# Kernel optimization log

Hardware: AMD Instinct MI355X
Metric: run time of the kernel (lower is better)

The kernel has to match this reference:

```python
import jax, jax.numpy as jnp
import numpy as np

N, M = 100000, 800000
F_IN, F_E, H = 64, 16, 64
T_NODE, T_EDGE = 2, 3
HEAD_DIM = 16.0


def setup_inputs() -> dict:
    key = jax.random.key(0)
    ks = jax.random.split(key, 16)
    inp = {
        "x": jax.random.normal(ks[0], (N, F_IN), jnp.float32),
        "edge_feat": jax.random.normal(ks[1], (M, F_E), jnp.float32),
        "node_type": jax.random.randint(ks[2], (N,), 0, T_NODE, jnp.int32),
        "edge_src": jax.random.randint(ks[3], (M,), 0, N, jnp.int32),
        "edge_dst": jax.random.randint(ks[4], (M,), 0, N, jnp.int32),
        "edge_type": jax.random.randint(ks[5], (M,), 0, T_EDGE, jnp.int32),
    }
    s_n = 1.0 / np.sqrt(F_IN)
    s_e = 1.0 / np.sqrt(F_E)
    for i, name in enumerate(["W1", "W2", "W3", "W4"]):
        inp[name] = jax.random.normal(ks[6 + i], (T_NODE, F_IN, H), jnp.float32) * s_n
        inp["b" + name[1]] = jax.random.normal(ks[10 + i], (T_NODE, H), jnp.float32) * 0.01
    inp["W5"] = jax.random.normal(ks[14], (T_EDGE, F_E, H), jnp.float32) * s_e
    inp["b5"] = jax.random.normal(ks[15], (T_EDGE, H), jnp.float32) * 0.01
    return inp


def _node_proj(x, W, b, node_type):
    # per-node-type linear: [T,F,H] weights, select row per node type
    p = jnp.einsum('nf,tfh->tnh', x, W) + b[:, None, :]      # [T,N,H]
    return jnp.take_along_axis(p, node_type[None, :, None], axis=0)[0]  # [N,H]


def reference(x, edge_feat, W1, b1, W2, b2, W3, b3, W4, b4, W5, b5,
              node_type, edge_src, edge_dst, edge_type):
    n = x.shape[0]
    h1 = _node_proj(x, W1, b1, node_type)
    h2 = _node_proj(x, W2, b2, node_type)
    h3 = _node_proj(x, W3, b3, node_type)
    h4 = _node_proj(x, W4, b4, node_type)
    # per-edge-type linear via weight gather (F_E is small)
    w5e = jnp.einsum('mf,mfh->mh', edge_feat, W5[edge_type]) + b5[edge_type]  # [M,H]
    # scalar attention logit per edge (w3_i . (w4_j + w5_ij)) / sqrt(head_dim)
    num = jnp.sum(h3[edge_dst] * (h4[edge_src] + w5e), axis=-1)  # [M]
    # softmax over a single scalar per edge == 1.0 exactly (faithful to source)
    score = jax.nn.softmax((num / jnp.sqrt(HEAD_DIM))[:, None], axis=-1)[:, 0]  # [M]
    msg = score[:, None] * (h2[edge_src] + w5e)                  # [M,H]
    out = h1 + jax.ops.segment_sum(msg, edge_dst, num_segments=n)
    return out
```

## Files before the change

### kernel.cpp

```cpp
#include <hip/hip_runtime.h>


#define CAP 16
#define OVF_CAP 32768

typedef __attribute__((ext_vector_type(8))) short short8;
typedef __attribute__((ext_vector_type(4))) float f32x4;

__device__ __forceinline__ float b2f(unsigned short u) {
    union { unsigned v; float f; } x; x.v = ((unsigned)u) << 16; return x.f;
}
__device__ __forceinline__ unsigned short f2b(float f) {
    union { float f; unsigned v; } x; x.f = f;
    unsigned u = x.v;
    unsigned r = (u + 0x7FFFu + ((u >> 16) & 1u)) >> 16;
    return (unsigned short)r;
}

__global__ __launch_bounds__(256) void k1_gemm_scatter(
    const float* __restrict__ x, const int* __restrict__ nt,
    const float* __restrict__ W1, const float* __restrict__ b1,
    const float* __restrict__ W2, const float* __restrict__ b2,
    const int* __restrict__ esrc, const int* __restrict__ edst,
    const int* __restrict__ etype,
    int* __restrict__ cnt32, int* __restrict__ ovfCnt,
    int4* __restrict__ ovf, int2* __restrict__ rec,
    float* __restrict__ out, unsigned short* __restrict__ h2b,
    int N, int M)
{
    __shared__ __align__(16) unsigned short sx[128 * 72];
    __shared__ __align__(16) unsigned short sw[4][64 * 72];
    __shared__ int snt[128];

    int tid = threadIdx.x;

    if (blockIdx.x & 1) {
        int e0 = (blockIdx.x >> 1) * 1024 + tid;
        int dd[4], ssrc[4], tty[4];
        bool v[4];
#pragma unroll
        for (int j = 0; j < 4; ++j) {
            int e = e0 + j * 256;
            v[j] = e < M;
            int ec = v[j] ? e : 0;
            dd[j]   = edst[ec];
            ssrc[j] = esrc[ec];
            tty[j]  = etype[ec];
        }
        int pos[4];
#pragma unroll
        for (int j = 0; j < 4; ++j)
            if (v[j]) pos[j] = atomicAdd(&cnt32[dd[j]], 1);
#pragma unroll
        for (int j = 0; j < 4; ++j) {
            if (!v[j]) continue;
            int packed = ssrc[j] | (tty[j] << 20);
            int e = e0 + j * 256;
            if (pos[j] < CAP) {
                rec[dd[j] * CAP + pos[j]] = make_int2(packed, e);
            } else {
                int slot = atomicAdd(ovfCnt, 1);
                if (slot < OVF_CAP) ovf[slot] = make_int4(packed, e, dd[j], 0);
            }
        }
        return;
    }

    int rowbase = (blockIdx.x >> 1) * 128;

    const float* Wm0 = W1;
    const float* Wm1 = W1 + 4096;
    const float* Wm2 = W2;
    const float* Wm3 = W2 + 4096;
#pragma unroll
    for (int j = 0; j < 4; ++j) {
        int k  = (tid >> 4) + j * 16;
        int n4 = (tid & 15) * 4;
        float4 w0 = *(const float4*)&Wm0[k * 64 + n4];
        float4 w1v = *(const float4*)&Wm1[k * 64 + n4];
        float4 w2v = *(const float4*)&Wm2[k * 64 + n4];
        float4 w3 = *(const float4*)&Wm3[k * 64 + n4];
        sw[0][(n4 + 0) * 72 + k] = f2b(w0.x);
        sw[0][(n4 + 1) * 72 + k] = f2b(w0.y);
        sw[0][(n4 + 2) * 72 + k] = f2b(w0.z);
        sw[0][(n4 + 3) * 72 + k] = f2b(w0.w);
        sw[1][(n4 + 0) * 72 + k] = f2b(w1v.x);
        sw[1][(n4 + 1) * 72 + k] = f2b(w1v.y);
        sw[1][(n4 + 2) * 72 + k] = f2b(w1v.z);
        sw[1][(n4 + 3) * 72 + k] = f2b(w1v.w);
        sw[2][(n4 + 0) * 72 + k] = f2b(w2v.x);
        sw[2][(n4 + 1) * 72 + k] = f2b(w2v.y);
        sw[2][(n4 + 2) * 72 + k] = f2b(w2v.z);
        sw[2][(n4 + 3) * 72 + k] = f2b(w2v.w);
        sw[3][(n4 + 0) * 72 + k] = f2b(w3.x);
        sw[3][(n4 + 1) * 72 + k] = f2b(w3.y);
        sw[3][(n4 + 2) * 72 + k] = f2b(w3.z);
        sw[3][(n4 + 3) * 72 + k] = f2b(w3.w);
    }

    if (tid < 128) {
        int r = rowbase + tid;
        snt[tid] = (r < N) ? nt[r] : 0;
    }

    int fr = (tid & 15) * 4;
    int ir = tid >> 4;
#pragma unroll
    for (int it = 0; it < 8; ++it) {
        int i = it * 16 + ir;
        int r = rowbase + i;
        float4 v = make_float4(0.f, 0.f, 0.f, 0.f);
        if (r < N) v = *(const float4*)&x[(size_t)r * 64 + fr];
        ushort4 p;
        p.x = f2b(v.x); p.y = f2b(v.y); p.z = f2b(v.z); p.w = f2b(v.w);
        *(ushort4*)&sx[i * 72 + fr] = p;
    }
    __syncthreads();

    int lane = tid & 63;
    int wid  = tid >> 6;
    int q    = lane >> 4;
    int cc   = lane & 15;
    int m0   = wid * 32;

    f32x4 acc[4][2][4];
#pragma unroll
    for (int mm = 0; mm < 4; ++mm)
#pragma unroll
        for (int s = 0; s < 2; ++s)
#pragma unroll
            for (int t = 0; t < 4; ++t)
                acc[mm][s][t] = (f32x4){0.f, 0.f, 0.f, 0.f};

#pragma unroll
    for (int k0 = 0; k0 < 64; k0 += 32) {
        int ko = k0 + q * 8;
        short8 af0 = *(short8*)&sx[(m0 + cc) * 72 + ko];
        short8 af1 = *(short8*)&sx[(m0 + 16 + cc) * 72 + ko];
#pragma unroll
        for (int mm = 0; mm < 4; ++mm)
#pragma unroll
            for (int t = 0; t < 4; ++t) {
                short8 bf = *(short8*)&sw[mm][(t * 16 + cc) * 72 + ko];
                acc[mm][0][t] = __builtin_amdgcn_mfma_f32_16x16x32_bf16(
                    af0, bf, acc[mm][0][t], 0, 0, 0);
                acc[mm][1][t] = __builtin_amdgcn_mfma_f32_16x16x32_bf16(
                    af1, bf, acc[mm][1][t], 0, 0, 0);
            }
    }

    float b1v[2][4], b2v[2][4];
#pragma unroll
    for (int ty = 0; ty < 2; ++ty)
#pragma unroll
        for (int t = 0; t < 4; ++t) {
            b1v[ty][t] = b1[ty * 64 + t * 16 + cc];
            b2v[ty][t] = b2[ty * 64 + t * 16 + cc];
        }

#pragma unroll
    for (int s = 0; s < 2; ++s)
#pragma unroll
        for (int reg = 0; reg < 4; ++reg) {
            int rl = m0 + s * 16 + q * 4 + reg;
            int r = rowbase + rl;
            if (r < N) {
                int ty = snt[rl];
#pragma unroll
                for (int t = 0; t < 4; ++t) {
                    float v1 = (ty ? acc[1][s][t][reg] : acc[0][s][t][reg])
                               + b1v[ty][t];
                    float v2 = (ty ? acc[3][s][t][reg] : acc[2][s][t][reg])
                               + b2v[ty][t];
                    out[(size_t)r * 64 + t * 16 + cc] = v1;
                    h2b[(size_t)r * 64 + t * 16 + cc] = f2b(v2);
                }
            }
        }
}

__global__ __launch_bounds__(256) void k2_gather(
    const float* __restrict__ ef, const int2* __restrict__ rec,
    const int* __restrict__ cnt32,
    const float* __restrict__ W5, const float* __restrict__ b5,
    const int4* __restrict__ ovf, const int* __restrict__ ovfCnt,
    const unsigned short* __restrict__ h2b, float* __restrict__ out,
    int N, int gatherBlocks, int ovfBlocks)
{
    __shared__ __align__(16) float sWt[64 * 52];
    __shared__ __align__(16) float sG[4][64];

    int tid = threadIdx.x;
    for (int i = tid; i < 3264; i += 256) {
        int j = i >> 6;
        int h = i & 63;
        float v = (j < 48) ? W5[i] : b5[i - 3072];
        sWt[h * 52 + j] = v;
    }
    if (tid < 64) sWt[tid * 52 + 51] = 0.f;
    __syncthreads();

    int lane = tid & 63;
    int wid = tid >> 6;

    if (blockIdx.x >= (unsigned)gatherBlocks) {
        int novf = min(*ovfCnt, OVF_CAP);
        int gw = (blockIdx.x - gatherBlocks) * 4 + wid;
        int nw = ovfBlocks * 4;
        for (int ri = gw; ri < novf; ri += nw) {
            int4 o = ovf[ri];
            int s = o.x & 0xFFFFF;
            int t = (unsigned)o.x >> 20;
            float acc = sWt[lane * 52 + 48 + t] +
                        b2f(h2b[((size_t)s << 6) | lane]);
            const float4* e4 = (const float4*)&ef[(size_t)o.y * 16];
            const float4* wt = (const float4*)&sWt[lane * 52 + t * 16];
#pragma unroll
            for (int f4 = 0; f4 < 4; ++f4) {
                float4 e = e4[f4];
                float4 w = wt[f4];
                acc = fmaf(e.x, w.x, acc);
                acc = fmaf(e.y, w.y, acc);
                acc = fmaf(e.z, w.z, acc);
                acc = fmaf(e.w, w.w, acc);
            }
            unsafeAtomicAdd(&out[(size_t)o.z * 64 + lane], acc);
        }
        return;
    }

    int d = blockIdx.x * 4 + wid;
    bool active = d < N;
    int deg = 0;
    if (active) deg = min(cnt32[d], CAP);
    unsigned base = (unsigned)d * CAP;

    int myt = (lane < 48) ? (lane >> 4) : (lane - 48);
    unsigned myf = lane & 15;
    bool fl = lane < 48;
    float accH = 0.f, accS = 0.f;
    float hLast = 0.f, vLast = 0.f;
    int tLast = -1;
    int degm1 = deg - 1;

    for (int i = 0; i < deg; i += 8) {
        int2 r[8];
#pragma unroll
        for (int j = 0; j < 8; ++j) {
            int ij = min(i + j, degm1);
            r[j] = rec[base + ij];
        }
        float hv[8], ev[8];
#pragma unroll
        for (int j = 0; j < 8; ++j) {
            unsigned s = (unsigned)r[j].x & 0xFFFFFu;
            hv[j] = b2f(h2b[((size_t)s << 6) | (unsigned)lane]);
            ev[j] = ef[((unsigned)r[j].y << 4) | myf];
        }
#pragma unroll
        for (int j = 0; j < 8; ++j) {
            int t = (int)((unsigned)r[j].x >> 20);
            float v = fl ? ev[j] : 1.0f;
            accH += hv[j];
            accS += (t == myt) ? v : 0.f;
            hLast = hv[j]; vLast = v; tLast = t;
        }
    }
    float fd = (float)(((deg + 7) & ~7) - deg);
    accH -= fd * hLast;
    accS -= (tLast == myt) ? fd * vLast : 0.f;

    sG[wid][lane] = accS;
    float rr = accH;
    const float4* g4 = (const float4*)sG[wid];
    const float4* w4 = (const float4*)&sWt[lane * 52];
#pragma unroll
    for (int j4 = 0; j4 < 13; ++j4) {
        float4 g = g4[j4];
        float4 w = w4[j4];
        rr = fmaf(g.x, w.x, rr);
        rr = fmaf(g.y, w.y, rr);
        rr = fmaf(g.z, w.z, rr);
        rr = fmaf(g.w, w.w, rr);
    }

    if (active)
        unsafeAtomicAdd(&out[((size_t)(unsigned)d << 6) | lane], rr);
}

extern "C" void kernel_launch(void* const* d_in, const int* in_sizes, int n_in,
                              void* d_out, int out_size, void* d_ws, size_t ws_size,
                              hipStream_t stream) {
    const float* x  = (const float*)d_in[0];
    const float* ef = (const float*)d_in[1];
    const int* nt   = (const int*)d_in[2];
    const int* es   = (const int*)d_in[3];
    const int* ed   = (const int*)d_in[4];
    const int* et   = (const int*)d_in[5];
    const float* W1 = (const float*)d_in[6];
    const float* b1 = (const float*)d_in[7];
    const float* W2 = (const float*)d_in[8];
    const float* b2 = (const float*)d_in[9];
    const float* W5 = (const float*)d_in[14];
    const float* b5 = (const float*)d_in[15];

    int N = in_sizes[2];
    int M = in_sizes[3];

    char* w = (char*)d_ws;
    size_t off = 0;
    unsigned short* h2b = (unsigned short*)(w + off); off += (size_t)N * 64 * 2;
    off = (off + 255) & ~(size_t)255;
    int2* rec = (int2*)(w + off); off += (size_t)N * CAP * 8;
    off = (off + 255) & ~(size_t)255;
    int4* ovf = (int4*)(w + off); off += (size_t)OVF_CAP * 16;
    off = (off + 255) & ~(size_t)255;
    int* ovfCnt = (int*)(w + off);
    int* cnt32  = (int*)(w + off + 64);
    size_t zeroBytes = 64 + (size_t)N * 4;

    float* out = (float*)d_out;

    hipMemsetAsync(ovfCnt, 0, zeroBytes, stream);

    int gemmBlocks    = (N + 127) / 128;
    int scatterBlocks = (M + 1023) / 1024;
    int gb1 = 2 * max(gemmBlocks, scatterBlocks);
    k1_gemm_scatter<<<gb1, 256, 0, stream>>>(
        x, nt, W1, b1, W2, b2, es, ed, et,
        cnt32, ovfCnt, ovf, rec, out, h2b, N, M);

    int gatherBlocks = (N + 3) / 4;
    int ovfBlocks = 32;
    k2_gather<<<gatherBlocks + ovfBlocks, 256, 0, stream>>>(
        ef, rec, cnt32, W5, b5, ovf, ovfCnt, h2b, out,
        N, gatherBlocks, ovfBlocks);
}
```

Measured before the change: 335.7 us.

## Move per-node W5 projection from gather kernel into separate MFMA GEMM kernel

The gather kernel no longer stages W5/b5 in shared memory or runs the per-node 52-wide dot product. It writes the per-type edge-feature sums to a workspace buffer, and a new third kernel multiplies them by W5 with bf16 MFMA, using a hi/lo split to keep fp32-like accuracy. This removes shared-memory setup and the LDS dot product from the gather blocks, which may raise occupancy. The cost is an extra launch plus an extra round trip through global memory for the N×52 buffer and a read-modify-write of out. The overflow path now reads W5 and b5 directly from global memory.

```diff
diff --git a/kernel.cpp b/kernel.cpp
--- a/kernel.cpp
+++ b/kernel.cpp
@@ -162,10 +162,10 @@
     for (int s = 0; s < 2; ++s)
 #pragma unroll
         for (int reg = 0; reg < 4; ++reg) {
-            int rl = m0 + s * 16 + q * 4 + reg;
-            int r = rowbase + rl;
+            int rl_ = m0 + s * 16 + q * 4 + reg;
+            int r = rowbase + rl_;
             if (r < N) {
-                int ty = snt[rl];
+                int ty = snt[rl_];
 #pragma unroll
                 for (int t = 0; t < 4; ++t) {
                     float v1 = (ty ? acc[1][s][t][reg] : acc[0][s][t][reg])
@@ -185,21 +185,10 @@
     const float* __restrict__ W5, const float* __restrict__ b5,
     const int4* __restrict__ ovf, const int* __restrict__ ovfCnt,
     const unsigned short* __restrict__ h2b, float* __restrict__ out,
+    float* __restrict__ sacc,
     int N, int gatherBlocks, int ovfBlocks)
 {
-    __shared__ __align__(16) float sWt[64 * 52];
-    __shared__ __align__(16) float sG[4][64];
-
     int tid = threadIdx.x;
-    for (int i = tid; i < 3264; i += 256) {
-        int j = i >> 6;
-        int h = i & 63;
-        float v = (j < 48) ? W5[i] : b5[i - 3072];
-        sWt[h * 52 + j] = v;
-    }
-    if (tid < 64) sWt[tid * 52 + 51] = 0.f;
-    __syncthreads();
-
     int lane = tid & 63;
     int wid = tid >> 6;
 
@@ -211,28 +200,20 @@
             int4 o = ovf[ri];
             int s = o.x & 0xFFFFF;
             int t = (unsigned)o.x >> 20;
-            float acc = sWt[lane * 52 + 48 + t] +
-                        b2f(h2b[((size_t)s << 6) | lane]);
-            const float4* e4 = (const float4*)&ef[(size_t)o.y * 16];
-            const float4* wt = (const float4*)&sWt[lane * 52 + t * 16];
-#pragma unroll
-            for (int f4 = 0; f4 < 4; ++f4) {
-                float4 e = e4[f4];
-                float4 w = wt[f4];
-                acc = fmaf(e.x, w.x, acc);
-                acc = fmaf(e.y, w.y, acc);
-                acc = fmaf(e.z, w.z, acc);
-                acc = fmaf(e.w, w.w, acc);
-            }
+            float acc = b5[t * 64 + lane] + b2f(h2b[((size_t)s << 6) | lane]);
+#pragma unroll
+            for (int f = 0; f < 16; ++f)
+                acc = fmaf(ef[(size_t)o.y * 16 + f],
+                           W5[(t * 16 + f) * 64 + lane], acc);
             unsafeAtomicAdd(&out[(size_t)o.z * 64 + lane], acc);
         }
         return;
     }
 
     int d = blockIdx.x * 4 + wid;
-    bool active = d < N;
-    int deg = 0;
-    if (active) deg = min(cnt32[d], CAP);
+    if (d >= N) return;
+
+    int dg = min(cnt32[d], CAP);
     unsigned base = (unsigned)d * CAP;
 
     int myt = (lane < 48) ? (lane >> 4) : (lane - 48);
@@ -241,13 +222,13 @@
     float accH = 0.f, accS = 0.f;
     float hLast = 0.f, vLast = 0.f;
     int tLast = -1;
-    int degm1 = deg - 1;
-
-    for (int i = 0; i < deg; i += 8) {
+    int dgm1 = dg - 1;
+
+    for (int i = 0; i < dg; i += 8) {
         int2 r[8];
 #pragma unroll
         for (int j = 0; j < 8; ++j) {
-            int ij = min(i + j, degm1);
+            int ij = min(i + j, dgm1);
             r[j] = rec[base + ij];
         }
         float hv[8], ev[8];
@@ -266,26 +247,119 @@
             hLast = hv[j]; vLast = v; tLast = t;
         }
     }
-    float fd = (float)(((deg + 7) & ~7) - deg);
+    float fd = (float)(((dg + 7) & ~7) - dg);
     accH -= fd * hLast;
     accS -= (tLast == myt) ? fd * vLast : 0.f;
 
-    sG[wid][lane] = accS;
-    float rr = accH;
-    const float4* g4 = (const float4*)sG[wid];
-    const float4* w4 = (const float4*)&sWt[lane * 52];
-#pragma unroll
-    for (int j4 = 0; j4 < 13; ++j4) {
-        float4 g = g4[j4];
-        float4 w = w4[j4];
-        rr = fmaf(g.x, w.x, rr);
-        rr = fmaf(g.y, w.y, rr);
-        rr = fmaf(g.z, w.z, rr);
-        rr = fmaf(g.w, w.w, rr);
-    }
-
-    if (active)
-        unsafeAtomicAdd(&out[((size_t)(unsigned)d << 6) | lane], rr);
+    if (lane < 52)
+        sacc[(size_t)d * 52 + lane] = accS;
+    if (dg > 0)
+        unsafeAtomicAdd(&out[((size_t)(unsigned)d << 6) | lane], accH);
+}
+
+__global__ __launch_bounds__(256) void k3_sacc_gemm(
+    const float* __restrict__ sacc, const float* __restrict__ W5,
+    const float* __restrict__ b5, float* __restrict__ out, int N)
+{
+    __shared__ __align__(16) unsigned short sa[128 * 136];
+    __shared__ __align__(16) unsigned short swt[64 * 136];
+
+    int tid = threadIdx.x;
+    int rowbase = blockIdx.x * 128;
+
+#pragma unroll
+    for (int k = 0; k < 7; ++k) {
+        int idx = tid + k * 256;
+        if (idx < 1664) {
+            int row = idx / 13;
+            int q4 = (idx - row * 13) * 4;
+            int d = rowbase + row;
+            float4 v = make_float4(0.f, 0.f, 0.f, 0.f);
+            if (d < N) v = *(const float4*)&sacc[(size_t)d * 52 + q4];
+            ushort4 hi, lo;
+            hi.x = f2b(v.x); lo.x = f2b(v.x - b2f(hi.x));
+            hi.y = f2b(v.y); lo.y = f2b(v.y - b2f(hi.y));
+            hi.z = f2b(v.z); lo.z = f2b(v.z - b2f(hi.z));
+            hi.w = f2b(v.w); lo.w = f2b(v.w - b2f(hi.w));
+            *(ushort4*)&sa[row * 136 + q4] = hi;
+            *(ushort4*)&sa[row * 136 + 52 + q4] = lo;
+        }
+    }
+    {
+        ushort4 z; z.x = 0; z.y = 0; z.z = 0; z.w = 0;
+#pragma unroll
+        for (int k = 0; k < 3; ++k) {
+            int idx = tid + k * 256;
+            int row = idx / 6;
+            int sp = (idx - row * 6) * 4;
+            *(ushort4*)&sa[row * 136 + 104 + sp] = z;
+        }
+#pragma unroll
+        for (int k = 0; k < 2; ++k) {
+            int idx = tid + k * 256;
+            if (idx < 384) {
+                int h = idx / 6;
+                int sp = (idx - h * 6) * 4;
+                *(ushort4*)&swt[h * 136 + 104 + sp] = z;
+            }
+        }
+    }
+#pragma unroll
+    for (int k = 0; k < 13; ++k) {
+        int idx = tid + k * 256;
+        int j = idx >> 6;
+        int h = idx & 63;
+        float wv = 0.f;
+        if (j < 48)      wv = W5[j * 64 + h];
+        else if (j < 51) wv = b5[(j - 48) * 64 + h];
+        unsigned short wb = f2b(wv);
+        swt[h * 136 + j] = wb;
+        swt[h * 136 + 52 + j] = wb;
+    }
+    __syncthreads();
+
+    int lane = tid & 63;
+    int wid  = tid >> 6;
+    int q    = lane >> 4;
+    int cc   = lane & 15;
+    int m0   = wid * 32;
+
+    f32x4 acc[2][4];
+#pragma unroll
+    for (int s = 0; s < 2; ++s)
+#pragma unroll
+        for (int t = 0; t < 4; ++t)
+            acc[s][t] = (f32x4){0.f, 0.f, 0.f, 0.f};
+
+#pragma unroll
+    for (int k0 = 0; k0 < 128; k0 += 32) {
+        int ko = k0 + q * 8;
+        short8 af0 = *(short8*)&sa[(m0 + cc) * 136 + ko];
+        short8 af1 = *(short8*)&sa[(m0 + 16 + cc) * 136 + ko];
+#pragma unroll
+        for (int t = 0; t < 4; ++t) {
+            short8 bf = *(short8*)&swt[(t * 16 + cc) * 136 + ko];
+            acc[0][t] = __builtin_amdgcn_mfma_f32_16x16x32_bf16(
+                af0, bf, acc[0][t], 0, 0, 0);
+            acc[1][t] = __builtin_amdgcn_mfma_f32_16x16x32_bf16(
+                af1, bf, acc[1][t], 0, 0, 0);
+        }
+    }
+
+#pragma unroll
+    for (int s = 0; s < 2; ++s)
+#pragma unroll
+        for (int reg = 0; reg < 4; ++reg) {
+            int rl_ = m0 + s * 16 + q * 4 + reg;
+            int r = rowbase + rl_;
+            if (r < N) {
+#pragma unroll
+                for (int t = 0; t < 4; ++t) {
+                    float* po = &out[(size_t)r * 64 + t * 16 + cc];
+                    *po += acc[s][t][reg];
+                }
+            }
+        }
 }
 
 extern "C" void kernel_launch(void* const* d_in, const int* in_sizes, int n_in,
@@ -315,6 +389,8 @@
     off = (off + 255) & ~(size_t)255;
     int4* ovf = (int4*)(w + off); off += (size_t)OVF_CAP * 16;
     off = (off + 255) & ~(size_t)255;
+    float* sacc = (float*)(w + off); off += (size_t)N * 52 * 4;
+    off = (off + 255) & ~(size_t)255;
     int* ovfCnt = (int*)(w + off);
     int* cnt32  = (int*)(w + off + 64);
     size_t zeroBytes = 64 + (size_t)N * 4;
@@ -333,6 +409,9 @@
     int gatherBlocks = (N + 3) / 4;
     int ovfBlocks = 32;
     k2_gather<<<gatherBlocks + ovfBlocks, 256, 0, stream>>>(
-        ef, rec, cnt32, W5, b5, ovf, ovfCnt, h2b, out,
+        ef, rec, cnt32, W5, b5, ovf, ovfCnt, h2b, out, sacc,
         N, gatherBlocks, ovfBlocks);
-}
+
+    int k3Blocks = (N + 127) / 128;
+    k3_sacc_gemm<<<k3Blocks, 256, 0, stream>>>(sacc, W5, b5, out, N);
+}
```

Result: faster. 314.3 us (-6.4%).
